# Kernel tuning notes

Hardware: AMD Instinct MI355X
Metric: run time of the kernel (lower is better)

Reference implementation:

```python
import jax, jax.numpy as jnp
import numpy as np

NP, P, NS = 5, 5, 15  # body parts, joints per part, segments per scale


def _gauss_forward(x):
    # x: (batch, nb_frames, joints=NP*P, coordinates, 1)
    b, T, J, C, _ = x.shape
    inp = x.reshape(b, T, NP, P, C, 1)
    # lengths of the 6 temporal windows: full, two halves, three thirds
    seg_lens = [T, T // 2, T - T // 2, T // 3, T // 3, T - 2 * (T // 3)]
    outs = []
    for L in seg_lens:
        nb_fr = L // NS
        # first NS-1 segments of nb_fr frames each, always starting at frame 0
        head = inp[:, :(NS - 1) * nb_fr].reshape(b, NS - 1, nb_fr, NP, P, C, 1)
        mu_h = head.mean(axis=2)                    # (b, NS-1, NP, P, C, 1)
        xc = head - mu_h[:, :, None]
        cov_h = jnp.einsum('bkfnpci,bkfnpdi->bknpcd', xc, xc) / nb_fr
        # last segment runs to the END of the full sequence (faithful to original)
        tail = inp[:, (NS - 1) * nb_fr:]
        rest = tail.shape[1]
        mu_t = tail.mean(axis=1)                    # (b, NP, P, C, 1)
        xt = tail - mu_t[:, None]
        cov_t = jnp.einsum('bfnpci,bfnpdi->bnpcd', xt, xt) / rest
        mu = jnp.concatenate([mu_h, mu_t[:, None]], axis=1)    # (b, NS, NP, P, C, 1)
        cov = jnp.concatenate([cov_h, cov_t[:, None]], axis=1)  # (b, NS, NP, P, C, C)
        # match torch layout (b, NP, NS, P, ...)
        mu = jnp.transpose(mu, (0, 2, 1, 3, 4, 5))
        cov = jnp.transpose(cov, (0, 2, 1, 3, 4, 5))
        muT = jnp.swapaxes(mu, -1, -2)
        elt00 = cov + mu @ muT                       # E[xx^T]
        ones = jnp.ones(mu.shape[:-2] + (1, 1), dtype=x.dtype)
        top = jnp.concatenate([elt00, mu], axis=-1)
        bot = jnp.concatenate([muT, ones], axis=-1)
        outs.append(jnp.concatenate([top, bot], axis=-2))
    # (b, 6, NP, NS, P, C+1, C+1)
    return jnp.stack(outs, axis=1)


def setup_inputs() -> dict:
    key = jax.random.key(0)
    x = jax.random.normal(key, (256, 2048, 25, 3, 1), dtype=jnp.float32)
    return {"x": x}


def reference(x):
    return _gauss_forward(x)
```

## Files before the change

kernel.cpp:

```cpp
#include <hip/hip_runtime.h>
#include <hip/hip_bf16.h>
#include <stdint.h>


#define NPIECE_MAX 64
struct Tab {
    int n;
    uint32_t p[NPIECE_MAX];
    uint32_t cr[45];
};

__global__ __launch_bounds__(256) void p1_kernel(const float* __restrict__ x,
                                                 float* __restrict__ ws, Tab tab) {
    __shared__ float sx[3760];
    int pc = blockIdx.x, b = blockIdx.y;
    uint32_t pk = tab.p[pc];
    int f0 = pk & 0xffff, L = (int)(pk >> 16);
    int w0 = f0 * 75;
    int base_f = w0 & ~3;
    int shift = w0 - base_f;
    int nv4 = (shift + L * 75 + 3) >> 2;
    const float4* src = (const float4*)(x + (size_t)b * 153600 + base_f);
    int tid = threadIdx.x;
    int wv = tid >> 6, ln = tid & 63;
    #pragma unroll
    for (int k = 0; k < 4; ++k) {
        int i = k * 256 + wv * 64 + ln;
        if (i < nv4) {
            __builtin_amdgcn_global_load_lds(
                (const __attribute__((address_space(1))) void*)(src + i),
                (__attribute__((address_space(3))) void*)(&sx[(size_t)(k * 256 + wv * 64) * 4]),
                16, 0, 0);
        }
    }
    __syncthreads();

    float s[9] = {0,0,0,0,0,0,0,0,0};
    if (tid < 250) {
        int j = tid % 25, ts = tid / 25;
        #pragma unroll 5
        for (int t = ts; t < L; t += 10) {
            const float* p = &sx[shift + t * 75 + j * 3];
            float a = p[0], bb = p[1], c = p[2];
            s[0]+=a;     s[1]+=bb;   s[2]+=c;
            s[3]+=a*a;   s[4]+=a*bb; s[5]+=a*c;
            s[6]+=bb*bb; s[7]+=bb*c; s[8]+=c*c;
        }
    }
    __syncthreads();
    if (tid < 250) {
        float* l = &sx[tid * 9];
        #pragma unroll
        for (int k = 0; k < 9; ++k) l[k] = s[k];
    }
    __syncthreads();
    if (tid < 225) {
        float v = 0.f;
        #pragma unroll
        for (int ts = 0; ts < 10; ++ts) v += sx[ts * 225 + tid];
        ws[((size_t)b * tab.n + pc) * 225 + tid] = v;
    }
}

#define IDXPK 0x9210287517640543ull

__global__ __launch_bounds__(256) void p2_kernel(const float* __restrict__ ws,
                                                 float* __restrict__ out, Tab tab) {
    __shared__ float sws[2520];
    __shared__ float red[2032];
    __shared__ float invn[45];
    int b = blockIdx.x, np = blockIdx.y;
    int tid = threadIdx.x;
    int n = tab.n;
    int tot = n * 45;
    const float* wb = ws + (size_t)b * n * 225 + np * 45;
    for (int i = tid; i < tot; i += 256) {
        int piece = i / 45, idx = i - piece * 45;
        sws[i] = wb[(size_t)piece * 225 + idx];
    }
    if (tid < 45) {
        int st = tid / 15, ch = tid - st * 15;
        const int nst[3] = {136, 68, 45};
        int ns = nst[st];
        int nfr = (ch == 14) ? (2048 - 14 * ns) : ns;
        invn[tid] = 1.0f / (float)nfr;
    }
    __syncthreads();

    for (int i = tid; i < 2025; i += 256) {
        int sc = i / 45, idx = i - sc * 45;
        uint32_t r = tab.cr[sc];
        int p0 = (int)(r & 0xffff), p1 = (int)(r >> 16);
        float v = 0.f;
        for (int p = p0; p < p1; ++p) v += sws[p * 45 + idx];
        red[i] = v;
    }
    __syncthreads();

    float4* ob4 = (float4*)(out + (size_t)b * 36000 + (size_t)np * 1200);
    for (int q = tid; q < 1800; q += 256) {
        int seg = q / 300;
        int q2  = q - seg * 300;
        int ch  = q2 / 20;
        int rem = q2 - ch * 20;
        int p   = rem >> 2;
        int r   = rem & 3;
        int st  = (seg == 0) ? 0 : (seg < 3) ? 1 : 2;
        int sc  = st * 15 + ch;
        float inv = invn[sc];
        const float* rb = &red[sc * 45 + p * 9];
        uint64_t pk = IDXPK >> (16 * r);
        float4 v;
        v.x = rb[(int)(pk       & 15)] * inv;
        v.y = rb[(int)((pk >> 4) & 15)] * inv;
        v.z = rb[(int)((pk >> 8) & 15)] * inv;
        v.w = (r == 3) ? 1.0f : rb[(int)((pk >> 12) & 15)] * inv;
        ob4[(size_t)seg * 1500 + q2] = v;
    }
}

__global__ __launch_bounds__(256) void gauss_fallback(const float* __restrict__ x,
                                                      float* __restrict__ out) {
    __shared__ float lds[2250];
    __shared__ float red[225];
    __shared__ float outm[400];
    int bid = blockIdx.x;
    int chunk = bid % 15;
    int tmp = bid / 15;
    int stype = tmp % 3;
    int b = tmp / 3;
    const int nbs[3] = {136, 68, 45};
    int ns = nbs[stype];
    int f0 = chunk * ns;
    int f1 = (chunk == 14) ? 2048 : (f0 + ns);
    float inv_n = 1.0f / (float)(f1 - f0);
    int tid = threadIdx.x;
    if (tid < 250) {
        int j = tid % 25, tsub = tid / 25;
        const float* base = x + (size_t)b * 153600 + j * 3;
        float s0=0.f,s1=0.f,s2=0.f,s3=0.f,s4=0.f,s5=0.f,s6=0.f,s7=0.f,s8=0.f;
        for (int t = f0 + tsub; t < f1; t += 10) {
            const float* p = base + (size_t)t * 75;
            float x0 = p[0], x1 = p[1], x2 = p[2];
            s0+=x0; s1+=x1; s2+=x2;
            s3+=x0*x0; s4+=x0*x1; s5+=x0*x2;
            s6+=x1*x1; s7+=x1*x2; s8+=x2*x2;
        }
        float* l = &lds[tid * 9];
        l[0]=s0; l[1]=s1; l[2]=s2; l[3]=s3; l[4]=s4; l[5]=s5; l[6]=s6; l[7]=s7; l[8]=s8;
    }
    __syncthreads();
    if (tid < 225) {
        float v = 0.f;
        #pragma unroll
        for (int ts = 0; ts < 10; ++ts) v += lds[ts * 225 + tid];
        red[tid] = v;
    }
    __syncthreads();
    if (tid < 25) {
        const float* r = &red[tid * 9];
        float mu0=r[0]*inv_n, mu1=r[1]*inv_n, mu2=r[2]*inv_n;
        float m00=r[3]*inv_n, m01=r[4]*inv_n, m02=r[5]*inv_n;
        float m11=r[6]*inv_n, m12=r[7]*inv_n, m22=r[8]*inv_n;
        float* o = &outm[tid * 16];
        o[0]=m00; o[1]=m01; o[2]=m02; o[3]=mu0;
        o[4]=m01; o[5]=m11; o[6]=m12; o[7]=mu1;
        o[8]=m02; o[9]=m12; o[10]=m22; o[11]=mu2;
        o[12]=mu0; o[13]=mu1; o[14]=mu2; o[15]=1.0f;
    }
    __syncthreads();
    int so0 = (stype == 0) ? 0 : (stype == 1) ? 1 : 3;
    int ndup = (stype == 0) ? 1 : (stype == 1) ? 2 : 3;
    int total = 400 * ndup;
    size_t obase = (size_t)b * 36000 + (size_t)chunk * 80;
    for (int idx = tid; idx < total; idx += 256) {
        int dup = idx % 400 == idx ? idx / 400 : idx / 400;
        int r = idx % 400;
        int np = r / 80;
        int rem = r % 80;
        out[obase + (size_t)(so0 + idx / 400) * 6000 + (size_t)np * 1200 + rem] = outm[r];
    }
}

static void build_tab(Tab& tab) {
    unsigned char isb[2049];
    for (int i = 0; i <= 2048; ++i) isb[i] = 0;
    isb[2048] = 1;
    for (int k = 1; k <= 14; ++k) { isb[45*k] = 1; isb[68*k] = 1; isb[136*k] = 1; }
    int n = 0, prev = 0;
    int pf0[NPIECE_MAX];
    for (int f = 1; f <= 2048; ++f) {
        if (!isb[f]) continue;
        int len = f - prev;
        int npc = (len + 49) / 50;
        int base = len / npc, rem = len % npc;
        int s = prev;
        for (int i = 0; i < npc && n < NPIECE_MAX; ++i) {
            int l = base + (i < rem ? 1 : 0);
            pf0[n] = s;
            tab.p[n++] = (uint32_t)(s | (l << 16));
            s += l;
        }
        prev = f;
    }
    tab.n = n;
    const int nst[3] = {136, 68, 45};
    for (int st = 0; st < 3; ++st) {
        int ns = nst[st];
        for (int c = 0; c < 15; ++c) {
            int a = c * ns, bnd = (c == 14) ? 2048 : (c + 1) * ns;
            int p0 = 0; while (p0 < n && pf0[p0] < a) ++p0;
            int p1 = p0; while (p1 < n && pf0[p1] < bnd) ++p1;
            tab.cr[st * 15 + c] = (uint32_t)(p0 | (p1 << 16));
        }
    }
}

extern "C" void kernel_launch(void* const* d_in, const int* in_sizes, int n_in,
                              void* d_out, int out_size, void* d_ws, size_t ws_size,
                              hipStream_t stream) {
    const float* x = (const float*)d_in[0];
    float* out = (float*)d_out;

    Tab tab;
    build_tab(tab);
    size_t need = (size_t)256 * tab.n * 225 * sizeof(float);

    if (ws_size >= need) {
        float* ws = (float*)d_ws;
        dim3 g1(tab.n, 256);
        p1_kernel<<<g1, 256, 0, stream>>>(x, ws, tab);
        dim3 g2(256, 5);
        p2_kernel<<<g2, 256, 0, stream>>>(ws, out, tab);
    } else {
        gauss_fallback<<<256 * 45, 256, 0, stream>>>(x, out);
    }
}
```

Measured before the change: 238.2 us.

## Use one block per boundary segment and load directly from global memory

New measurement: 237.8 us. Within noise of the previous version (-0.1%).

```diff
diff --git a/kernel.cpp b/kernel.cpp
--- a/kernel.cpp
+++ b/kernel.cpp
@@ -1,72 +1,51 @@
 #include <hip/hip_runtime.h>
-#include <hip/hip_bf16.h>
 #include <stdint.h>
 
 
-#define NPIECE_MAX 64
+#define NSEG_MAX 40
+#define IDXPK 0x9210287517640543ull
+
 struct Tab {
     int n;
-    uint32_t p[NPIECE_MAX];
+    uint32_t p[NSEG_MAX];
     uint32_t cr[45];
 };
 
 __global__ __launch_bounds__(256) void p1_kernel(const float* __restrict__ x,
                                                  float* __restrict__ ws, Tab tab) {
-    __shared__ float sx[3760];
+    __shared__ float lds[2250];
     int pc = blockIdx.x, b = blockIdx.y;
     uint32_t pk = tab.p[pc];
     int f0 = pk & 0xffff, L = (int)(pk >> 16);
-    int w0 = f0 * 75;
-    int base_f = w0 & ~3;
-    int shift = w0 - base_f;
-    int nv4 = (shift + L * 75 + 3) >> 2;
-    const float4* src = (const float4*)(x + (size_t)b * 153600 + base_f);
     int tid = threadIdx.x;
-    int wv = tid >> 6, ln = tid & 63;
-    #pragma unroll
-    for (int k = 0; k < 4; ++k) {
-        int i = k * 256 + wv * 64 + ln;
-        if (i < nv4) {
-            __builtin_amdgcn_global_load_lds(
-                (const __attribute__((address_space(1))) void*)(src + i),
-                (__attribute__((address_space(3))) void*)(&sx[(size_t)(k * 256 + wv * 64) * 4]),
-                16, 0, 0);
+
+    float s0=0.f,s1=0.f,s2=0.f,s3=0.f,s4=0.f,s5=0.f,s6=0.f,s7=0.f,s8=0.f;
+    if (tid < 250) {
+        int fslot = tid / 25;
+        const float* q = x + (size_t)b * 153600 + (size_t)f0 * 75 + tid * 3;
+        int nk = (L - fslot + 9) / 10;
+        #pragma unroll 3
+        for (int k = 0; k < nk; ++k, q += 750) {
+            float a = q[0], bb = q[1], c = q[2];
+            s0 += a;      s1 += bb;     s2 += c;
+            s3 += a * a;  s4 += a * bb; s5 += a * c;
+            s6 += bb * bb; s7 += bb * c; s8 += c * c;
         }
-    }
-    __syncthreads();
-
-    float s[9] = {0,0,0,0,0,0,0,0,0};
-    if (tid < 250) {
-        int j = tid % 25, ts = tid / 25;
-        #pragma unroll 5
-        for (int t = ts; t < L; t += 10) {
-            const float* p = &sx[shift + t * 75 + j * 3];
-            float a = p[0], bb = p[1], c = p[2];
-            s[0]+=a;     s[1]+=bb;   s[2]+=c;
-            s[3]+=a*a;   s[4]+=a*bb; s[5]+=a*c;
-            s[6]+=bb*bb; s[7]+=bb*c; s[8]+=c*c;
-        }
-    }
-    __syncthreads();
-    if (tid < 250) {
-        float* l = &sx[tid * 9];
-        #pragma unroll
-        for (int k = 0; k < 9; ++k) l[k] = s[k];
+        float* l = &lds[tid * 9];
+        l[0]=s0; l[1]=s1; l[2]=s2; l[3]=s3; l[4]=s4; l[5]=s5; l[6]=s6; l[7]=s7; l[8]=s8;
     }
     __syncthreads();
     if (tid < 225) {
         float v = 0.f;
         #pragma unroll
-        for (int ts = 0; ts < 10; ++ts) v += sx[ts * 225 + tid];
+        for (int fs = 0; fs < 10; ++fs) v += lds[fs * 225 + tid];
         ws[((size_t)b * tab.n + pc) * 225 + tid] = v;
     }
 }
-
-#define IDXPK 0x9210287517640543ull
 
 __global__ __launch_bounds__(256) void p2_kernel(const float* __restrict__ ws,
                                                  float* __restrict__ out, Tab tab) {
-    __shared__ float sws[2520];
+    __shared__ float sws[1620];
     __shared__ float red[2032];
     __shared__ float invn[45];
     int b = blockIdx.x, np = blockIdx.y;
@@ -109,12 +88,12 @@
         int sc  = st * 15 + ch;
         float inv = invn[sc];
         const float* rb = &red[sc * 45 + p * 9];
-        uint64_t pk = IDXPK >> (16 * r);
+        uint64_t pkk = IDXPK >> (16 * r);
         float4 v;
-        v.x = rb[(int)(pk       & 15)] * inv;
-        v.y = rb[(int)((pk >> 4) & 15)] * inv;
-        v.z = rb[(int)((pk >> 8) & 15)] * inv;
-        v.w = (r == 3) ? 1.0f : rb[(int)((pk >> 12) & 15)] * inv;
+        v.x = rb[(int)(pkk & 15)] * inv;
+        v.y = rb[(int)((pkk >> 4) & 15)] * inv;
+        v.z = rb[(int)((pkk >> 8) & 15)] * inv;
+        v.w = (r == 3) ? 1.0f : rb[(int)((pkk >> 12) & 15)] * inv;
         ob4[(size_t)seg * 1500 + q2] = v;
     }
 }
@@ -174,11 +153,11 @@
     int total = 400 * ndup;
     size_t obase = (size_t)b * 36000 + (size_t)chunk * 80;
     for (int idx = tid; idx < total; idx += 256) {
-        int dup = idx % 400 == idx ? idx / 400 : idx / 400;
+        int dup = idx / 400;
         int r = idx % 400;
         int np = r / 80;
         int rem = r % 80;
-        out[obase + (size_t)(so0 + idx / 400) * 6000 + (size_t)np * 1200 + rem] = outm[r];
+        out[obase + (size_t)(so0 + dup) * 6000 + (size_t)np * 1200 + rem] = outm[r];
     }
 }
 
@@ -186,21 +165,13 @@
     unsigned char isb[2049];
     for (int i = 0; i <= 2048; ++i) isb[i] = 0;
     isb[2048] = 1;
-    for (int k = 1; k <= 14; ++k) { isb[45*k] = 1; isb[68*k] = 1; isb[136*k] = 1; }
+    for (int k = 1; k <= 14; ++k) { isb[45 * k] = 1; isb[68 * k] = 1; isb[136 * k] = 1; }
     int n = 0, prev = 0;
-    int pf0[NPIECE_MAX];
+    int pf0[NSEG_MAX];
     for (int f = 1; f <= 2048; ++f) {
         if (!isb[f]) continue;
-        int len = f - prev;
-        int npc = (len + 49) / 50;
-        int base = len / npc, rem = len % npc;
-        int s = prev;
-        for (int i = 0; i < npc && n < NPIECE_MAX; ++i) {
-            int l = base + (i < rem ? 1 : 0);
-            pf0[n] = s;
-            tab.p[n++] = (uint32_t)(s | (l << 16));
-            s += l;
-        }
+        pf0[n] = prev;
+        tab.p[n++] = (uint32_t)(prev | ((f - prev) << 16));
         prev = f;
     }
     tab.n = n;
@@ -221,7 +192,6 @@
                               hipStream_t stream) {
     const float* x = (const float*)d_in[0];
     float* out = (float*)d_out;
-
     Tab tab;
     build_tab(tab);
     size_t need = (size_t)256 * tab.n * 225 * sizeof(float);
```
